# Kernel optimization log

Measured on AMD Instinct MI355X. Metric: run time of the kernel, lower is better.

## Reference

```python
import jax, jax.numpy as jnp
import numpy as np

N_NODES = 50000
N_EDGES = 640000
D = 128
N_RELS = 16
N_NTYPES = 8


def setup_inputs() -> dict:
    key = jax.random.key(0)
    ks = jax.random.split(key, 9)
    return {
        "feats": jax.random.normal(ks[0], (N_NODES, D), dtype=jnp.float32),
        "W_edge": jax.random.normal(ks[1], (N_RELS, D, D), dtype=jnp.float32) / np.sqrt(D),
        "b_edge": jax.random.normal(ks[2], (N_RELS, D), dtype=jnp.float32) * 0.02,
        "W_node": jax.random.normal(ks[3], (N_NTYPES, D, D), dtype=jnp.float32) / np.sqrt(D),
        "b_node": jax.random.normal(ks[4], (N_NTYPES, D), dtype=jnp.float32) * 0.02,
        "src": jax.random.randint(ks[5], (N_EDGES,), 0, N_NODES, dtype=jnp.int32),
        "dst": jax.random.randint(ks[6], (N_EDGES,), 0, N_NODES, dtype=jnp.int32),
        "ntypes": jax.random.randint(ks[7], (N_NODES,), 0, N_NTYPES, dtype=jnp.int32),
        "etypes": jax.random.randint(ks[8], (N_EDGES,), 0, N_RELS, dtype=jnp.int32),
    }


def reference(feats, W_edge, b_edge, W_node, b_node, src, dst, ntypes, etypes):
    N, d = feats.shape
    T = W_edge.shape[0]
    # Per-relation linear applied to all nodes once: [T, N, out]; then gather per edge.
    hW = jnp.einsum('nd,tdf->tnf', feats, W_edge) + b_edge[:, None, :]
    msg = hW[etypes, src]  # [E, out]
    # Per-(dst-node, edge-type) in-degree counts (one_hot count normalization).
    seg = dst * T + etypes  # [E]
    counts = jax.ops.segment_sum(jnp.ones(msg.shape[0], dtype=msg.dtype), seg,
                                 num_segments=N * T)  # [N*T]
    msg = msg / counts[seg][:, None]
    # Scatter-sum messages into destination nodes (zero for isolated nodes).
    agg = jax.ops.segment_sum(msg, dst, num_segments=N)  # [N, out]
    # Type-conditional node transform + residual message + activation.
    hN = jnp.einsum('nd,tdf->tnf', feats, W_node) + b_node[:, None, :]  # [Tn, N, out]
    out = hN[ntypes, jnp.arange(N)] + agg
    return jax.nn.relu(out)
```

## Files before the change

### kernel.cpp

```cpp
#include <hip/hip_runtime.h>
#include <hip/hip_bf16.h>
#include <stdint.h>


#define D 128
#define TRELS 16
#define NTYPES 8

typedef __bf16 bf16x8 __attribute__((ext_vector_type(8)));
typedef float f32x4 __attribute__((ext_vector_type(4)));
typedef unsigned int u32x4 __attribute__((ext_vector_type(4)));

__device__ __forceinline__ unsigned short f2bf(float f) {
  union { float f; unsigned u; } v; v.f = f;
  unsigned u = v.u;
  return (unsigned short)((u + 0x7FFFu + ((u >> 16) & 1u)) >> 16);
}
__device__ __forceinline__ float bf2f(unsigned short h) {
  union { unsigned u; float f; } v; v.u = ((unsigned)h) << 16;
  return v.f;
}
__device__ __forceinline__ void bfpair(unsigned u, float& lo, float& hi) {
  union { unsigned u; float f; } a, b;
  a.u = u << 16; b.u = u & 0xffff0000u;
  lo = a.f; hi = b.f;
}

__global__ void prep_k(const float* __restrict__ feats,
                       const float* __restrict__ We,
                       const float* __restrict__ Wn,
                       unsigned short* __restrict__ featsbf,
                       unsigned short* __restrict__ WeT,
                       unsigned short* __restrict__ WnT,
                       int nfeat) {
  int idx = blockIdx.x * 256 + threadIdx.x;
  if (idx < nfeat) { featsbf[idx] = f2bf(feats[idx]); return; }
  idx -= nfeat;
  if (idx < TRELS * D * D) {
    int t = idx >> 14, rem = idx & 16383;
    int n = rem >> 7, k = rem & 127;
    WeT[idx] = f2bf(We[t * 16384 + k * 128 + n]);
    return;
  }
  idx -= TRELS * D * D;
  if (idx < NTYPES * D * D) {
    int t = idx >> 14, rem = idx & 16383;
    int n = rem >> 7, k = rem & 127;
    WnT[idx] = f2bf(Wn[t * 16384 + k * 128 + n]);
  }
}

__global__ void hist_k(const int* __restrict__ dst, const int* __restrict__ etypes,
                       const int* __restrict__ ntypes, int E, int N,
                       int* __restrict__ cnt, int* __restrict__ nhist) {
  __shared__ int sh_n[NTYPES];
  int tid = threadIdx.x;
  if (tid < NTYPES) sh_n[tid] = 0;
  __syncthreads();
  int g = blockIdx.x * 256 + tid;
  if (g < E) atomicAdd(&cnt[dst[g] * TRELS + etypes[g]], 1);
  if (g < N) atomicAdd(&sh_n[ntypes[g]], 1);
  __syncthreads();
  if (tid < NTYPES && sh_n[tid]) atomicAdd(&nhist[tid], sh_n[tid]);
}

__global__ void scan1_k(const int* __restrict__ cnt, int* __restrict__ doff,
                        int* __restrict__ bsum, int N) {
  __shared__ int sd[256];
  int b = blockIdx.x, tid = threadIdx.x;
  int base = b * 1024 + tid * 4;
  int v[4]; int tot = 0;
  for (int j = 0; j < 4; ++j) {
    int i = base + j;
    int dg = 0;
    if (i < N) {
      const int* row = cnt + i * TRELS;
#pragma unroll
      for (int et = 0; et < TRELS; ++et) dg += row[et];
    }
    v[j] = tot; tot += dg;
  }
  sd[tid] = tot;
  __syncthreads();
  for (int off = 1; off < 256; off <<= 1) {
    int t = (tid >= off) ? sd[tid - off] : 0;
    __syncthreads();
    sd[tid] += t;
    __syncthreads();
  }
  int excl = sd[tid] - tot;
  for (int j = 0; j < 4; ++j) {
    int i = base + j;
    if (i < N) doff[i] = excl + v[j];
  }
  if (tid == 255) bsum[b] = sd[255];
}

__global__ void scan2_k(int* __restrict__ misc, int* __restrict__ bsum, int nb) {
  if (threadIdx.x != 0) return;
  int run = 0;
  for (int b = 0; b < nb; ++b) { int t = bsum[b]; bsum[b] = run; run += t; }
  int* noff = misc; int* ntb = misc + 9; int* ncur = misc + 18; int* nhist = misc + 26;
  int s = 0, ts = 0;
  for (int t = 0; t < NTYPES; ++t) {
    noff[t] = s; ncur[t] = s; ntb[t] = ts;
    s += nhist[t]; ts += (nhist[t] + 127) >> 7;
  }
  noff[NTYPES] = s; ntb[NTYPES] = ts;
}

__global__ void scan3_k(int* __restrict__ doff, int* __restrict__ dcur,
                        const int* __restrict__ bsum, int N, int E) {
  int b = blockIdx.x, tid = threadIdx.x;
  int add = bsum[b];
  int base = b * 1024 + tid * 4;
  for (int j = 0; j < 4; ++j) {
    int i = base + j;
    if (i < N) { int o = doff[i] + add; doff[i] = o; dcur[i] = o; }
  }
  if (b == 0 && tid == 0) doff[N] = E;
}

__global__ void scatter_k(const int* __restrict__ src, const int* __restrict__ dst,
                          const int* __restrict__ etypes, const int* __restrict__ ntypes,
                          int E, int N, int* __restrict__ misc,
                          int* __restrict__ dcur,
                          int* __restrict__ edst, int* __restrict__ nsorted) {
  __shared__ int lc_n[NTYPES], lb_n[NTYPES];
  int tid = threadIdx.x;
  if (tid < NTYPES) lc_n[tid] = 0;
  __syncthreads();
  int g = blockIdx.x * 256 + tid;
  if (g < E) {
    int d = dst[g];
    int pos = atomicAdd(&dcur[d], 1);
    edst[pos] = src[g] * TRELS + etypes[g];
  }
  int tn = -1, idn = 0;
  if (g < N) { tn = ntypes[g]; idn = atomicAdd(&lc_n[tn], 1); }
  __syncthreads();
  if (tid < NTYPES && lc_n[tid]) lb_n[tid] = atomicAdd(&misc[18 + tid], lc_n[tid]);
  __syncthreads();
  if (g < N) nsorted[lb_n[tn] + idn] = g;
}

__global__ __launch_bounds__(256) void hw_gemm_k(
    const unsigned short* __restrict__ featsbf,
    const unsigned short* __restrict__ WeT,
    unsigned short* __restrict__ hW, int N, int mtiles) {
  __shared__ unsigned char Asm[128 * 264];
  int tid = threadIdx.x;

  int G = mtiles * 16;
  int q = G >> 3, rmod = G & 7;
  int xcd = blockIdx.x & 7, bidx = blockIdx.x >> 3;
  int wrk = (xcd < rmod) ? (xcd * (q + 1) + bidx)
                         : (rmod * (q + 1) + (xcd - rmod) * q + bidx);
  int tile = wrk >> 4;
  int et = wrk & 15;

  int lane = tid & 63, w = tid >> 6;
  int m = lane & 15, qd = lane >> 4;
  int rw = (w & 1) * 64, cw = (w >> 1) * 64;

  const unsigned short* WB = WeT + et * (D * D);
  bf16x8 bfr[4][4];
#pragma unroll
  for (int ks = 0; ks < 4; ++ks)
#pragma unroll
    for (int j = 0; j < 4; ++j)
      bfr[ks][j] = *reinterpret_cast<const bf16x8*>(WB + (cw + j * 16 + m) * D + ks * 32 + qd * 8);

  int r = tid >> 1, h = tid & 1;
  int row = tile * 128 + r;
  if (row < N) {
    const u32x4* gp = reinterpret_cast<const u32x4*>(featsbf + (size_t)row * D);
#pragma unroll
    for (int cc = 0; cc < 8; ++cc) {
      int c = h * 8 + cc;
      *reinterpret_cast<u32x4*>(&Asm[r * 256 + ((c ^ (r & 7)) << 4)]) = gp[c];
    }
  }
  __syncthreads();

  f32x4 acc[4][4];
#pragma unroll
  for (int i = 0; i < 4; ++i)
#pragma unroll
    for (int j = 0; j < 4; ++j) acc[i][j] = (f32x4){0.f, 0.f, 0.f, 0.f};

#pragma unroll
  for (int ks = 0; ks < 4; ++ks) {
    bf16x8 a[4];
#pragma unroll
    for (int i = 0; i < 4; ++i) {
      int rr = rw + i * 16 + m;
      int c = ks * 4 + qd;
      a[i] = *reinterpret_cast<const bf16x8*>(&Asm[rr * 256 + ((c ^ (rr & 7)) << 4)]);
    }
#pragma unroll
    for (int i = 0; i < 4; ++i)
#pragma unroll
      for (int j = 0; j < 4; ++j)
        acc[i][j] = __builtin_amdgcn_mfma_f32_16x16x32_bf16(a[i], bfr[ks][j], acc[i][j], 0, 0, 0);
  }

  __syncthreads();
  unsigned short* Cs = reinterpret_cast<unsigned short*>(Asm);
#pragma unroll
  for (int i = 0; i < 4; ++i)
#pragma unroll
    for (int j = 0; j < 4; ++j)
#pragma unroll
      for (int reg = 0; reg < 4; ++reg) {
        int rr = rw + i * 16 + qd * 4 + reg;
        Cs[rr * 132 + cw + j * 16 + m] = f2bf(acc[i][j][reg]);
      }
  __syncthreads();
  char* gout = (char*)(hW + ((size_t)et * N + (size_t)tile * 128) * D);
#pragma unroll
  for (int cp = 0; cp < 8; ++cp) {
    int o = cp * 4096 + tid * 16;
    int rloc = o >> 8;
    if (tile * 128 + rloc < N) {
      u32x4 v = *reinterpret_cast<const u32x4*>(&Asm[rloc * 264 + (o & 255)]);
      __builtin_nontemporal_store(v, reinterpret_cast<u32x4*>(gout + o));
    }
  }
}

__global__ __launch_bounds__(256) void agg_k(
    const unsigned short* __restrict__ hW,
    const float* __restrict__ b_edge,
    const int* __restrict__ cnt,
    const int* __restrict__ doff, const int* __restrict__ edst,
    float* __restrict__ agg, int N) {
  int tid = threadIdx.x;
  int lane = tid & 63, w = tid >> 6;
  int d = blockIdx.x * 4 + w;
  if (d >= N) return;

  int cv = 0;
  if (lane < TRELS) cv = cnt[d * TRELS + lane];
  float invl = (cv > 0) ? 1.0f / (float)cv : 0.0f;

  int g = lane >> 4;
  int sub = lane & 15;

  int start = doff[d], end = doff[d + 1];
  float acc[8];
#pragma unroll
  for (int z = 0; z < 8; ++z) acc[z] = 0.f;

  for (int base = start; base < end; base += 64) {
    int key = 0;
    if (base + lane < end) key = edst[base + lane];
    int nchunk = end - base; if (nchunk > 64) nchunk = 64;
#pragma unroll 2
    for (int j = 0; j < nchunk; j += 4) {
      int rr = j + g;
      int k = __shfl(key, rr, 64);
      float inv = __shfl(invl, k & 15, 64);
      if (rr < nchunk) {
        const unsigned short* hp =
            hW + ((size_t)(k & 15) * N + (size_t)(k >> 4)) * D + sub * 8;
        u32x4 hv = *reinterpret_cast<const u32x4*>(hp);
        float lo, hi;
        bfpair(hv.x, lo, hi); acc[0] += inv * lo; acc[1] += inv * hi;
        bfpair(hv.y, lo, hi); acc[2] += inv * lo; acc[3] += inv * hi;
        bfpair(hv.z, lo, hi); acc[4] += inv * lo; acc[5] += inv * hi;
        bfpair(hv.w, lo, hi); acc[6] += inv * lo; acc[7] += inv * hi;
      }
    }
  }

#pragma unroll
  for (int z = 0; z < 8; ++z) {
    acc[z] += __shfl_xor(acc[z], 16, 64);
    acc[z] += __shfl_xor(acc[z], 32, 64);
  }

  int cb = sub * 8 + (g & 1) * 4;
  f32x4 res = { acc[(g & 1) * 4 + 0], acc[(g & 1) * 4 + 1],
                acc[(g & 1) * 4 + 2], acc[(g & 1) * 4 + 3] };
#pragma unroll
  for (int et = 0; et < TRELS; ++et) {
    int c = __shfl(cv, et, 64);
    if (c > 0) {
      f32x4 b4 = *reinterpret_cast<const f32x4*>(b_edge + et * D + cb);
#pragma unroll
      for (int z = 0; z < 4; ++z) res[z] += b4[z];
    }
  }
  if (g < 2)
    *reinterpret_cast<f32x4*>(agg + (size_t)d * D + cb) = res;
}

__global__ __launch_bounds__(256) void node_gemm_k(
    const unsigned short* __restrict__ featsbf,
    const unsigned short* __restrict__ WnT,
    const float* __restrict__ b_node,
    const int* __restrict__ nsorted, const int* __restrict__ misc,
    const float* __restrict__ agg,
    float* __restrict__ out) {
  __shared__ unsigned char Asm[128 * 264];
  __shared__ int sm_node[128];
  __shared__ int s_ntb[9];
  int tid = threadIdx.x;
  if (tid < 9) s_ntb[tid] = misc[9 + tid];
  __syncthreads();
  int bid = blockIdx.x;
  if (bid >= s_ntb[8]) return;
  int t = 0;
  while (bid >= s_ntb[t + 1]) ++t;
  int tile = bid - s_ntb[t];
  int noff_t = misc[t];
  int cntT = misc[t + 1] - noff_t;

  int lane = tid & 63, w = tid >> 6;
  int m = lane & 15, q = lane >> 4;
  int rw = (w & 1) * 64, cw = (w >> 1) * 64;

  const unsigned short* WB = WnT + t * (D * D);
  bf16x8 bfr[4][4];
#pragma unroll
  for (int ks = 0; ks < 4; ++ks)
#pragma unroll
    for (int j = 0; j < 4; ++j)
      bfr[ks][j] = *reinterpret_cast<const bf16x8*>(WB + (cw + j * 16 + m) * D + ks * 32 + q * 8);

  int r = tid >> 1, h = tid & 1;
  int gidx = tile * 128 + r;
  bool rv = gidx < cntT;
  int node = 0;
  if (rv) node = nsorted[noff_t + gidx];
  if (h == 0) sm_node[r] = rv ? node : -1;
  if (rv) {
    const u32x4* gp = reinterpret_cast<const u32x4*>(featsbf + (size_t)node * D);
#pragma unroll
    for (int cc = 0; cc < 8; ++cc) {
      int c = h * 8 + cc;
      *reinterpret_cast<u32x4*>(&Asm[r * 256 + ((c ^ (r & 7)) << 4)]) = gp[c];
    }
  }
  __syncthreads();

  f32x4 acc[4][4];
#pragma unroll
  for (int i = 0; i < 4; ++i)
#pragma unroll
    for (int j = 0; j < 4; ++j) acc[i][j] = (f32x4){0.f, 0.f, 0.f, 0.f};

#pragma unroll
  for (int ks = 0; ks < 4; ++ks) {
    bf16x8 a[4];
#pragma unroll
    for (int i = 0; i < 4; ++i) {
      int rr = rw + i * 16 + m;
      int c = ks * 4 + q;
      a[i] = *reinterpret_cast<const bf16x8*>(&Asm[rr * 256 + ((c ^ (rr & 7)) << 4)]);
    }
#pragma unroll
    for (int i = 0; i < 4; ++i)
#pragma unroll
      for (int j = 0; j < 4; ++j)
        acc[i][j] = __builtin_amdgcn_mfma_f32_16x16x32_bf16(a[i], bfr[ks][j], acc[i][j], 0, 0, 0);
  }

  const float* bnp = b_node + t * D;
  float* Cf = reinterpret_cast<float*>(Asm);
  __syncthreads();
#pragma unroll
  for (int half = 0; half < 2; ++half) {
    if ((w & 1) == half) {
#pragma unroll
      for (int i = 0; i < 4; ++i)
#pragma unroll
        for (int j = 0; j < 4; ++j)
#pragma unroll
          for (int reg = 0; reg < 4; ++reg) {
            int rl = i * 16 + q * 4 + reg;
            Cf[rl * 132 + cw + j * 16 + m] = acc[i][j][reg];
          }
    }
    __syncthreads();
#pragma unroll
    for (int cp = 0; cp < 8; ++cp) {
      int o = cp * 4096 + tid * 16;
      int rl = o >> 9;
      int nd = sm_node[half * 64 + rl];
      if (nd >= 0) {
        int col = (o & 511) >> 2;
        f32x4 c = *reinterpret_cast<const f32x4*>((char*)Cf + rl * 528 + (o & 511));
        f32x4 a = *reinterpret_cast<const f32x4*>(agg + (size_t)nd * D + col);
        f32x4 b4 = *reinterpret_cast<const f32x4*>(bnp + col);
        f32x4 res;
#pragma unroll
        for (int z = 0; z < 4; ++z) res[z] = fmaxf(c[z] + a[z] + b4[z], 0.f);
        *reinterpret_cast<f32x4*>(out + (size_t)nd * D + col) = res;
      }
    }
    __syncthreads();
  }
}

static inline size_t align256(size_t x) { return (x + 255) & ~(size_t)255; }

extern "C" void kernel_launch(void* const* d_in, const int* in_sizes, int n_in,
                              void* d_out, int out_size, void* d_ws, size_t ws_size,
                              hipStream_t stream) {
  const float* feats  = (const float*)d_in[0];
  const float* W_edge = (const float*)d_in[1];
  const float* b_edge = (const float*)d_in[2];
  const float* W_node = (const float*)d_in[3];
  const float* b_node = (const float*)d_in[4];
  const int* src    = (const int*)d_in[5];
  const int* dst    = (const int*)d_in[6];
  const int* ntypes = (const int*)d_in[7];
  const int* etypes = (const int*)d_in[8];
  int N = in_sizes[0] / D;
  int E = in_sizes[5];

  char* ws = (char*)d_ws;
  size_t o_cnt  = 0;
  size_t o_misc = align256(o_cnt + (size_t)N * TRELS * 4);
  size_t zend   = align256(o_misc + 512);
  size_t o_doff = zend;
  size_t o_dcur = align256(o_doff + (size_t)(N + 1) * 4);
  size_t o_edst = align256(o_dcur + (size_t)N * 4);
  size_t o_ns   = align256(o_edst + (size_t)E * 4);
  size_t o_fb   = align256(o_ns + (size_t)N * 4);
  size_t o_we   = align256(o_fb + (size_t)N * D * 2);
  size_t o_wn   = align256(o_we + (size_t)TRELS * D * D * 2);
  size_t o_agg  = align256(o_wn + (size_t)NTYPES * D * D * 2);
  size_t o_hw   = align256(o_agg + (size_t)N * D * 4);

  int* cnt = (int*)(ws + o_cnt);
  int* misc = (int*)(ws + o_misc);
  int* doff = (int*)(ws + o_doff);
  int* dcur = (int*)(ws + o_dcur);
  int* edst = (int*)(ws + o_edst);
  int* nsorted = (int*)(ws + o_ns);
  unsigned short* featsbf = (unsigned short*)(ws + o_fb);
  unsigned short* WeT = (unsigned short*)(ws + o_we);
  unsigned short* WnT = (unsigned short*)(ws + o_wn);
  float* agg = (float*)(ws + o_agg);
  unsigned short* hW = (unsigned short*)(ws + o_hw);
  int* bsum = misc + 64;

  (void)hipMemsetAsync(ws, 0, zend, stream);

  int nfeat = N * D;
  int ptot = nfeat + TRELS * D * D + NTYPES * D * D;
  prep_k<<<(ptot + 255) / 256, 256, 0, stream>>>(feats, W_edge, W_node, featsbf, WeT, WnT, nfeat);

  int hgrid = ((E > N ? E : N) + 255) / 256;
  hist_k<<<hgrid, 256, 0, stream>>>(dst, etypes, ntypes, E, N, cnt, misc + 26);

  int nb = (N + 1023) / 1024;
  scan1_k<<<nb, 256, 0, stream>>>(cnt, doff, bsum, N);
  scan2_k<<<1, 64, 0, stream>>>(misc, bsum, nb);
  scan3_k<<<nb, 256, 0, stream>>>(doff, dcur, bsum, N, E);

  scatter_k<<<hgrid, 256, 0, stream>>>(src, dst, etypes, ntypes, E, N, misc, dcur, edst, nsorted);

  int mtiles = (N + 127) / 128;
  hw_gemm_k<<<mtiles * 16, 256, 0, stream>>>(featsbf, WeT, hW, N, mtiles);

  agg_k<<<(N + 3) / 4, 256, 0, stream>>>(hW, b_edge, cnt, doff, edst, agg, N);

  int ngrid = mtiles + NTYPES;
  node_gemm_k<<<ngrid, 256, 0, stream>>>(featsbf, WnT, b_node, nsorted, misc, agg, (float*)d_out);
}
```

Baseline: 347.4 us.

## Fuse prep and histogram kernels, vectorize casts, tile weight transpose, two nodes per warp

```diff
diff --git a/kernel.cpp b/kernel.cpp
--- a/kernel.cpp
+++ b/kernel.cpp
@@ -16,48 +16,65 @@
   unsigned u = v.u;
   return (unsigned short)((u + 0x7FFFu + ((u >> 16) & 1u)) >> 16);
 }
-__device__ __forceinline__ float bf2f(unsigned short h) {
-  union { unsigned u; float f; } v; v.u = ((unsigned)h) << 16;
-  return v.f;
-}
 __device__ __forceinline__ void bfpair(unsigned u, float& lo, float& hi) {
   union { unsigned u; float f; } a, b;
   a.u = u << 16; b.u = u & 0xffff0000u;
   lo = a.f; hi = b.f;
 }
 
-__global__ void prep_k(const float* __restrict__ feats,
-                       const float* __restrict__ We,
-                       const float* __restrict__ Wn,
-                       unsigned short* __restrict__ featsbf,
-                       unsigned short* __restrict__ WeT,
-                       unsigned short* __restrict__ WnT,
-                       int nfeat) {
-  int idx = blockIdx.x * 256 + threadIdx.x;
-  if (idx < nfeat) { featsbf[idx] = f2bf(feats[idx]); return; }
-  idx -= nfeat;
-  if (idx < TRELS * D * D) {
-    int t = idx >> 14, rem = idx & 16383;
-    int n = rem >> 7, k = rem & 127;
-    WeT[idx] = f2bf(We[t * 16384 + k * 128 + n]);
+__global__ void prep_hist_k(const float* __restrict__ feats,
+                            const float* __restrict__ We,
+                            const float* __restrict__ Wn,
+                            const int* __restrict__ dst, const int* __restrict__ etypes,
+                            const int* __restrict__ ntypes,
+                            unsigned short* __restrict__ featsbf,
+                            unsigned short* __restrict__ WeT,
+                            unsigned short* __restrict__ WnT,
+                            int* __restrict__ cnt, int* __restrict__ nhist,
+                            int N, int E, int nfeat, int fb, int wb) {
+  __shared__ unsigned short Ts[64][65];
+  __shared__ int sh_n[NTYPES];
+  int b = blockIdx.x;
+  int tid = threadIdx.x;
+  if (b < fb) {
+    int i = (b * 256 + tid) * 8;
+    if (i + 8 <= nfeat) {
+      const f32x4* fp = reinterpret_cast<const f32x4*>(feats + i);
+      f32x4 a = fp[0], c = fp[1];
+      u32x4 pk;
+      pk[0] = (unsigned)f2bf(a[0]) | ((unsigned)f2bf(a[1]) << 16);
+      pk[1] = (unsigned)f2bf(a[2]) | ((unsigned)f2bf(a[3]) << 16);
+      pk[2] = (unsigned)f2bf(c[0]) | ((unsigned)f2bf(c[1]) << 16);
+      pk[3] = (unsigned)f2bf(c[2]) | ((unsigned)f2bf(c[3]) << 16);
+      *reinterpret_cast<u32x4*>(featsbf + i) = pk;
+    }
     return;
   }
-  idx -= TRELS * D * D;
-  if (idx < NTYPES * D * D) {
-    int t = idx >> 14, rem = idx & 16383;
-    int n = rem >> 7, k = rem & 127;
-    WnT[idx] = f2bf(Wn[t * 16384 + k * 128 + n]);
-  }
-}
-
-__global__ void hist_k(const int* __restrict__ dst, const int* __restrict__ etypes,
-                       const int* __restrict__ ntypes, int E, int N,
-                       int* __restrict__ cnt, int* __restrict__ nhist) {
-  __shared__ int sh_n[NTYPES];
-  int tid = threadIdx.x;
+  b -= fb;
+  if (b < wb) {
+    int mat = b >> 2, tq = b & 3;
+    const float* Ws = (mat < TRELS) ? (We + (size_t)mat * D * D)
+                                    : (Wn + (size_t)(mat - TRELS) * D * D);
+    unsigned short* Wd = (mat < TRELS) ? (WeT + (size_t)mat * D * D)
+                                       : (WnT + (size_t)(mat - TRELS) * D * D);
+    int k0 = (tq >> 1) * 64, n0 = (tq & 1) * 64;
+#pragma unroll
+    for (int p = 0; p < 16; ++p) {
+      int kr = (tid >> 6) + p * 4, cn = tid & 63;
+      Ts[kr][cn] = f2bf(Ws[(k0 + kr) * D + n0 + cn]);
+    }
+    __syncthreads();
+#pragma unroll
+    for (int p = 0; p < 16; ++p) {
+      int nr = (tid >> 6) + p * 4, ck = tid & 63;
+      Wd[(n0 + nr) * D + k0 + ck] = Ts[ck][nr];
+    }
+    return;
+  }
+  b -= wb;
   if (tid < NTYPES) sh_n[tid] = 0;
   __syncthreads();
-  int g = blockIdx.x * 256 + tid;
+  int g = b * 256 + tid;
   if (g < E) atomicAdd(&cnt[dst[g] * TRELS + etypes[g]], 1);
   if (g < N) atomicAdd(&sh_n[ntypes[g]], 1);
   __syncthreads();
@@ -163,7 +180,7 @@
   int m = lane & 15, qd = lane >> 4;
   int rw = (w & 1) * 64, cw = (w >> 1) * 64;
 
-  const unsigned short* WB = WeT + et * (D * D);
+  const unsigned short* WB = WeT + (size_t)et * (D * D);
   bf16x8 bfr[4][4];
 #pragma unroll
   for (int ks = 0; ks < 4; ++ks)
@@ -224,7 +241,7 @@
     int rloc = o >> 8;
     if (tile * 128 + rloc < N) {
       u32x4 v = *reinterpret_cast<const u32x4*>(&Asm[rloc * 264 + (o & 255)]);
-      __builtin_nontemporal_store(v, reinterpret_cast<u32x4*>(gout + o));
+      *reinterpret_cast<u32x4*>(gout + o) = v;
     }
   }
 }
@@ -237,63 +254,93 @@
     float* __restrict__ agg, int N) {
   int tid = threadIdx.x;
   int lane = tid & 63, w = tid >> 6;
-  int d = blockIdx.x * 4 + w;
-  if (d >= N) return;
+  int d0 = blockIdx.x * 8 + w * 2;
+  if (d0 >= N) return;
+  int d1 = d0 + 1;
+  bool has1 = d1 < N;
 
   int cv = 0;
-  if (lane < TRELS) cv = cnt[d * TRELS + lane];
+  if (lane < 32) {
+    int dd = d0 + (lane >> 4);
+    if (dd < N) cv = cnt[dd * TRELS + (lane & 15)];
+  }
   float invl = (cv > 0) ? 1.0f / (float)cv : 0.0f;
 
-  int g = lane >> 4;
-  int sub = lane & 15;
-
-  int start = doff[d], end = doff[d + 1];
-  float acc[8];
-#pragma unroll
-  for (int z = 0; z < 8; ++z) acc[z] = 0.f;
-
-  for (int base = start; base < end; base += 64) {
-    int key = 0;
-    if (base + lane < end) key = edst[base + lane];
-    int nchunk = end - base; if (nchunk > 64) nchunk = 64;
+  int g = lane >> 4, sub = lane & 15;
+
+  int s0 = doff[d0];
+  int e0 = doff[d0 + 1];
+  int e1 = has1 ? doff[d0 + 2] : e0;
+  int n0 = e0 - s0, n1 = e1 - e0;
+  int nmax = (n0 > n1) ? n0 : n1;
+
+  float acc0[8], acc1[8];
+#pragma unroll
+  for (int z = 0; z < 8; ++z) { acc0[z] = 0.f; acc1[z] = 0.f; }
+
+  for (int base = 0; base < nmax; base += 64) {
+    int key0 = 0, key1 = 0;
+    if (base + lane < n0) key0 = edst[s0 + base + lane];
+    if (base + lane < n1) key1 = edst[e0 + base + lane];
+    int c0 = n0 - base; c0 = (c0 > 64) ? 64 : ((c0 < 0) ? 0 : c0);
+    int c1 = n1 - base; c1 = (c1 > 64) ? 64 : ((c1 < 0) ? 0 : c1);
+    int cm = (c0 > c1) ? c0 : c1;
 #pragma unroll 2
-    for (int j = 0; j < nchunk; j += 4) {
+    for (int j = 0; j < cm; j += 4) {
       int rr = j + g;
-      int k = __shfl(key, rr, 64);
-      float inv = __shfl(invl, k & 15, 64);
-      if (rr < nchunk) {
+      int k0 = __shfl(key0, rr, 64);
+      int k1 = __shfl(key1, rr, 64);
+      float iv0 = __shfl(invl, k0 & 15, 64);
+      float iv1 = __shfl(invl, 16 + (k1 & 15), 64);
+      if (rr < c0) {
         const unsigned short* hp =
-            hW + ((size_t)(k & 15) * N + (size_t)(k >> 4)) * D + sub * 8;
+            hW + ((size_t)(k0 & 15) * N + (size_t)(k0 >> 4)) * D + sub * 8;
         u32x4 hv = *reinterpret_cast<const u32x4*>(hp);
         float lo, hi;
-        bfpair(hv.x, lo, hi); acc[0] += inv * lo; acc[1] += inv * hi;
-        bfpair(hv.y, lo, hi); acc[2] += inv * lo; acc[3] += inv * hi;
-        bfpair(hv.z, lo, hi); acc[4] += inv * lo; acc[5] += inv * hi;
-        bfpair(hv.w, lo, hi); acc[6] += inv * lo; acc[7] += inv * hi;
+        bfpair(hv.x, lo, hi); acc0[0] += iv0 * lo; acc0[1] += iv0 * hi;
+        bfpair(hv.y, lo, hi); acc0[2] += iv0 * lo; acc0[3] += iv0 * hi;
+        bfpair(hv.z, lo, hi); acc0[4] += iv0 * lo; acc0[5] += iv0 * hi;
+        bfpair(hv.w, lo, hi); acc0[6] += iv0 * lo; acc0[7] += iv0 * hi;
       }
+      if (rr < c1) {
+        const unsigned short* hp =
+            hW + ((size_t)(k1 & 15) * N + (size_t)(k1 >> 4)) * D + sub * 8;
+        u32x4 hv = *reinterpret_cast<const u32x4*>(hp);
+        float lo, hi;
+        bfpair(hv.x, lo, hi); acc1[0] += iv1 * lo; acc1[1] += iv1 * hi;
+        bfpair(hv.y, lo, hi); acc1[2] += iv1 * lo; acc1[3] += iv1 * hi;
+        bfpair(hv.z, lo, hi); acc1[4] += iv1 * lo; acc1[5] += iv1 * hi;
+        bfpair(hv.w, lo, hi); acc1[6] += iv1 * lo; acc1[7] += iv1 * hi;
+      }
     }
   }
 
 #pragma unroll
   for (int z = 0; z < 8; ++z) {
-    acc[z] += __shfl_xor(acc[z], 16, 64);
-    acc[z] += __shfl_xor(acc[z], 32, 64);
+    acc0[z] += __shfl_xor(acc0[z], 16, 64);
+    acc0[z] += __shfl_xor(acc0[z], 32, 64);
+    acc1[z] += __shfl_xor(acc1[z], 16, 64);
+    acc1[z] += __shfl_xor(acc1[z], 32, 64);
   }
 
   int cb = sub * 8 + (g & 1) * 4;
-  f32x4 res = { acc[(g & 1) * 4 + 0], acc[(g & 1) * 4 + 1],
-                acc[(g & 1) * 4 + 2], acc[(g & 1) * 4 + 3] };
+  bool lo2 = (g < 2);
+  f32x4 res;
+#pragma unroll
+  for (int z = 0; z < 4; ++z) res[z] = lo2 ? acc0[(g & 1) * 4 + z] : acc1[(g & 1) * 4 + z];
+  int srcl = lo2 ? 0 : 16;
 #pragma unroll
   for (int et = 0; et < TRELS; ++et) {
-    int c = __shfl(cv, et, 64);
-    if (c > 0) {
+    int cc = __shfl(cv, srcl + et, 64);
+    if (cc > 0) {
       f32x4 b4 = *reinterpret_cast<const f32x4*>(b_edge + et * D + cb);
 #pragma unroll
       for (int z = 0; z < 4; ++z) res[z] += b4[z];
     }
   }
-  if (g < 2)
-    *reinterpret_cast<f32x4*>(agg + (size_t)d * D + cb) = res;
+  int dT = lo2 ? d0 : d1;
+  if (lo2 || has1)
+    *reinterpret_cast<f32x4*>(agg + (size_t)dT * D + cb) = res;
 }
 
 __global__ __launch_bounds__(256) void node_gemm_k(
@@ -451,23 +498,23 @@
   (void)hipMemsetAsync(ws, 0, zend, stream);
 
   int nfeat = N * D;
-  int ptot = nfeat + TRELS * D * D + NTYPES * D * D;
-  prep_k<<<(ptot + 255) / 256, 256, 0, stream>>>(feats, W_edge, W_node, featsbf, WeT, WnT, nfeat);
-
-  int hgrid = ((E > N ? E : N) + 255) / 256;
-  hist_k<<<hgrid, 256, 0, stream>>>(dst, etypes, ntypes, E, N, cnt, misc + 26);
+  int fb = (nfeat / 8 + 255) / 256;
+  int wb = (TRELS + NTYPES) * 4;
+  int hb = ((E > N ? E : N) + 255) / 256;
+  prep_hist_k<<<fb + wb + hb, 256, 0, stream>>>(feats, W_edge, W_node,
+      dst, etypes, ntypes, featsbf, WeT, WnT, cnt, misc + 26, N, E, nfeat, fb, wb);
 
   int nb = (N + 1023) / 1024;
   scan1_k<<<nb, 256, 0, stream>>>(cnt, doff, bsum, N);
   scan2_k<<<1, 64, 0, stream>>>(misc, bsum, nb);
   scan3_k<<<nb, 256, 0, stream>>>(doff, dcur, bsum, N, E);
 
-  scatter_k<<<hgrid, 256, 0, stream>>>(src, dst, etypes, ntypes, E, N, misc, dcur, edst, nsorted);
+  scatter_k<<<hb, 256, 0, stream>>>(src, dst, etypes, ntypes, E, N, misc, dcur, edst, nsorted);
 
   int mtiles = (N + 127) / 128;
   hw_gemm_k<<<mtiles * 16, 256, 0, stream>>>(featsbf, WeT, hW, N, mtiles);
 
-  agg_k<<<(N + 3) / 4, 256, 0, stream>>>(hW, b_edge, cnt, doff, edst, agg, N);
+  agg_k<<<(N + 7) / 8, 256, 0, stream>>>(hW, b_edge, cnt, doff, edst, agg, N);
 
   int ngrid = mtiles + NTYPES;
   node_gemm_k<<<ngrid, 256, 0, stream>>>(featsbf, WnT, b_node, nsorted, misc, agg, (float*)d_out);
```

Result: slower. 359.8 us (+3.6%).
